# Performance work log

Measured on AMD Instinct MI355X. Metric: run time of the kernel, lower is better.

## Reference

```python
import jax, jax.numpy as jnp
import numpy as np

B, H, W, C = 32, 64, 64, 128
WIN, NH, HD = 8, 4, 32
WW = WIN * WIN          # 64 tokens per window
BW = B * (H // WIN) * (W // WIN)  # 2048 windows
LN_EPS = 1e-5


def _ln(x, w, b):
    mu = jnp.mean(x, -1, keepdims=True)
    var = jnp.var(x, -1, keepdims=True)
    return (x - mu) * jax.lax.rsqrt(var + LN_EPS) * w + b


def setup_inputs() -> dict:
    key = jax.random.key(0)
    ks = jax.random.split(key, 24)
    n = lambda i, s, sc=0.02: jax.random.normal(ks[i], s, jnp.float32) * sc
    return {
        "out_dense_b": n(0, (C,)),
        "out_dense_w": n(1, (C, C)),
        "rel_coords_table": jax.random.uniform(ks[2], (1, 2 * WIN - 1, 2 * WIN - 1, 2), jnp.float32, -1.0, 1.0),
        "cpb0_b": n(3, (512,)),
        "cpb0_w": n(4, (512, 2)),
        "cpb2_w": n(5, (NH, 512)),
        "value_b": n(6, (C,)),
        "value_w": n(7, (C, C)),
        "logit_scale": jnp.full((NH, 1, 1), jnp.log(10.0), jnp.float32),
        "inter_b": n(8, (4 * C,)),
        "inter_w": n(9, (4 * C, C)),
        "ln_after_b": n(10, (C,)),
        "ln_after_w": jnp.ones((C,), jnp.float32),
        "ln_before_b": n(11, (C,)),
        "ln_before_w": jnp.ones((C,), jnp.float32),
        "ffn_out_b": n(12, (C,)),
        "ffn_out_w": n(13, (C, 4 * C)),
        "ds_norm_b": n(14, (2 * C,)),
        "ds_norm_w": jnp.ones((2 * C,), jnp.float32),
        "ds_red_w": n(15, (2 * C, 4 * C)),
        "embeddings_3": jax.random.normal(ks[16], (B, H * W, C), jnp.float32),
        "hidden_states_windows": jax.random.normal(ks[17], (BW, WW, C), jnp.float32),
        "key_layer": jax.random.normal(ks[18], (BW, NH, WW, HD), jnp.float32),
        "query_layer": jax.random.normal(ks[19], (BW, NH, WW, HD), jnp.float32),
        "rel_pos_index": jax.random.randint(ks[20], (WW, WW), 0, (2 * WIN - 1) ** 2).astype(jnp.int64),
    }


def reference(out_dense_b, out_dense_w, rel_coords_table, cpb0_b, cpb0_w, cpb2_w,
              value_b, value_w, logit_scale, inter_b, inter_w,
              ln_after_b, ln_after_w, ln_before_b, ln_before_w,
              ffn_out_b, ffn_out_w, ds_norm_b, ds_norm_w, ds_red_w,
              embeddings_3, hidden_states_windows, key_layer, query_layer,
              rel_pos_index):
    # value projection -> [BW, NH, WW, HD]
    v = (hidden_states_windows @ value_w.T + value_b).reshape(BW, WW, NH, HD).transpose(0, 2, 1, 3)
    # cosine attention
    qn = query_layer / jnp.maximum(jnp.linalg.norm(query_layer, axis=-1, keepdims=True), 1e-12)
    kn = key_layer / jnp.maximum(jnp.linalg.norm(key_layer, axis=-1, keepdims=True), 1e-12)
    scale = jnp.exp(jnp.minimum(logit_scale, jnp.log(100.0)))  # [NH,1,1]
    attn = jnp.einsum("bhqd,bhkd->bhqk", qn, kn) * scale
    # continuous position bias MLP
    t = rel_coords_table.reshape(-1, 2)                       # [(2w-1)^2, 2]
    bias_table = jax.nn.relu(t @ cpb0_w.T + cpb0_b) @ cpb2_w.T  # [(2w-1)^2, NH]
    bias = bias_table[rel_pos_index.reshape(-1)].reshape(WW, WW, NH).transpose(2, 0, 1)
    bias = 16.0 * jax.nn.sigmoid(bias)
    attn = jax.nn.softmax(attn + bias[None], axis=-1)
    ctx = jnp.einsum("bhqk,bhkd->bhqd", attn, v).transpose(0, 2, 1, 3).reshape(BW, WW, C)
    attn_out = ctx @ out_dense_w.T + out_dense_b
    # window reverse -> [B, H*W, C]
    x = attn_out.reshape(B, H // WIN, W // WIN, WIN, WIN, C)
    x = x.transpose(0, 1, 3, 2, 4, 5).reshape(B, H * W, C)
    # res-post-norm residual
    hs = embeddings_3 + _ln(x, ln_before_w, ln_before_b)
    # MLP with res-post-norm
    ffn = jax.nn.gelu(hs @ inter_w.T + inter_b, approximate=False)
    ffn = ffn @ ffn_out_w.T + ffn_out_b
    layer_out = hs + _ln(ffn, ln_after_w, ln_after_b)
    # patch merging downsample
    xm = layer_out.reshape(B, H, W, C)
    merged = jnp.concatenate(
        [xm[:, 0::2, 0::2], xm[:, 1::2, 0::2], xm[:, 0::2, 1::2], xm[:, 1::2, 1::2]],
        axis=-1,
    ).reshape(B, (H // 2) * (W // 2), 4 * C)
    red = merged @ ds_red_w.T
    return _ln(red, ds_norm_w, ds_norm_b)
```

## Files before the change

kernel.cpp:

```cpp
#include <hip/hip_runtime.h>
#include <hip/hip_bf16.h>

typedef __attribute__((ext_vector_type(4))) float f4;
typedef __attribute__((ext_vector_type(8))) short s8;
typedef __attribute__((ext_vector_type(4))) short s4;

__device__ __forceinline__ short f2bf(float f){
  __hip_bfloat16 h = __float2bfloat16(f);
  return __builtin_bit_cast(short, h);
}
__device__ __forceinline__ float bf2f(short h){
  unsigned u = ((unsigned)(unsigned short)h) << 16;
  return __builtin_bit_cast(float, u);
}
__device__ __forceinline__ f4 mfma16(s8 a, s8 b, f4 c){
  return __builtin_amdgcn_mfma_f32_16x16x32_bf16(a, b, c, 0, 0, 0);
}
__device__ __forceinline__ s8 cfrag(const float* p){
  f4 a = *(const f4*)p; f4 b = *(const f4*)(p + 4);
  s8 t = {f2bf(a[0]), f2bf(a[1]), f2bf(a[2]), f2bf(a[3]),
          f2bf(b[0]), f2bf(b[1]), f2bf(b[2]), f2bf(b[3])};
  return t;
}
__device__ __forceinline__ s8 nfrag(const float* p){
  f4 a = *(const f4*)p; f4 b = *(const f4*)(p + 4);
  float ss = a[0]*a[0]+a[1]*a[1]+a[2]*a[2]+a[3]*a[3]
           + b[0]*b[0]+b[1]*b[1]+b[2]*b[2]+b[3]*b[3];
  ss += __shfl_xor(ss, 16); ss += __shfl_xor(ss, 32);
  float f = 1.0f / fmaxf(sqrtf(ss), 1e-12f);
  s8 t = {f2bf(a[0]*f), f2bf(a[1]*f), f2bf(a[2]*f), f2bf(a[3]*f),
          f2bf(b[0]*f), f2bf(b[1]*f), f2bf(b[2]*f), f2bf(b[3]*f)};
  return t;
}
#define SWZ(row) ((((row) ^ ((row) >> 3)) & 7) << 3)

__global__ __launch_bounds__(256) void k_prep(
    const float* __restrict__ vw, const float* __restrict__ ow,
    const float* __restrict__ iw, const float* __restrict__ fw,
    const float* __restrict__ dw, const float* __restrict__ tbl,
    const float* __restrict__ c0b, const float* __restrict__ c0w,
    const float* __restrict__ c2w, const int* __restrict__ rpi,
    short* __restrict__ wsw, float* __restrict__ bias)
{
  if (blockIdx.x < 288) {
    int e0 = (blockIdx.x * 256 + threadIdx.x) * 4;
#pragma unroll
    for (int i = 0; i < 4; ++i) {
      int e = e0 + i;
      float v;
      if (e < 16384) v = vw[e];
      else if (e < 32768) v = ow[e - 16384];
      else if (e < 98304) v = iw[e - 32768];
      else if (e < 163840) v = fw[e - 98304];
      else v = dw[e - 163840];
      wsw[e] = f2bf(v);
    }
    return;
  }
  __shared__ float tb[900];
  __shared__ float cw[1024], cb[512], c2l[2048];
  __shared__ int orAcc;
  int tid = threadIdx.x;
  if (tid == 0) orAcc = 0;
  for (int i = tid; i < 1024; i += 256) cw[i] = c0w[i];
  for (int i = tid; i < 512;  i += 256) cb[i] = c0b[i];
  for (int i = tid; i < 2048; i += 256) c2l[i] = c2w[i];
  __syncthreads();
  int my = 0;
  for (int i = tid; i < 2048; i += 256) my |= rpi[2 * i + 1];
  atomicOr(&orAcc, my);
  if (tid < 225) {
    float t0 = tbl[tid * 2 + 0], t1 = tbl[tid * 2 + 1];
    float s0 = 0.f, s1 = 0.f, s2 = 0.f, s3 = 0.f;
    for (int j = 0; j < 512; ++j) {
      float hv = fmaxf(t0 * cw[j * 2] + t1 * cw[j * 2 + 1] + cb[j], 0.f);
      s0 += hv * c2l[j];
      s1 += hv * c2l[512 + j];
      s2 += hv * c2l[1024 + j];
      s3 += hv * c2l[1536 + j];
    }
    tb[tid * 4 + 0] = s0; tb[tid * 4 + 1] = s1;
    tb[tid * 4 + 2] = s2; tb[tid * 4 + 3] = s3;
  }
  __syncthreads();
  bool i64 = (orAcc == 0);
#pragma unroll
  for (int it = 0; it < 64; ++it) {
    int e = it * 256 + tid;
    int rem = e & 4095;
    int h = e >> 12;
    int idx = i64 ? rpi[2 * rem] : rpi[rem];
    float v = tb[idx * 4 + h];
    bias[e] = 16.f / (1.f + __expf(-v));
  }
}

__global__ __launch_bounds__(256, 3) void k_attn(
    const float* __restrict__ hswp, const float* __restrict__ qg,
    const float* __restrict__ kg, const float* __restrict__ lsc,
    const float* __restrict__ vb, const short* __restrict__ wvb,
    const float* __restrict__ bias, short* __restrict__ ctx)
{
  __shared__ short lds[16384];
  const int bw = blockIdx.x, tid = threadIdx.x;
  const int lane = tid & 63, h = tid >> 6;
  const int r16 = lane & 15, b4 = lane >> 4;

  const float* qp = qg + ((size_t)bw * 4 + h) * 2048;
  const float* kp = kg + ((size_t)bw * 4 + h) * 2048;
  const float* hp = hswp + (size_t)bw * 8192;

  s8 qf[4], kf[4];
#pragma unroll
  for (int t = 0; t < 4; ++t) qf[t] = nfrag(qp + (t * 16 + r16) * 32 + b4 * 8);
#pragma unroll
  for (int t = 0; t < 4; ++t) kf[t] = nfrag(kp + (t * 16 + r16) * 32 + b4 * 8);

  {
    int row = tid >> 2, c0 = (tid & 3) * 32;
    const float* src = hp + row * 128 + c0;
    short* dst = &lds[row * 136 + c0];
#pragma unroll
    for (int j = 0; j < 4; ++j)
      *(s8*)(dst + j * 8) = cfrag(src + j * 8);
  }
  __syncthreads();

  f4 vac[2][4];
#pragma unroll
  for (int ct = 0; ct < 2; ++ct)
#pragma unroll
    for (int tt = 0; tt < 4; ++tt) vac[ct][tt] = (f4){0.f, 0.f, 0.f, 0.f};
#pragma unroll
  for (int ks = 0; ks < 4; ++ks) {
    s8 bfr[4];
#pragma unroll
    for (int tt = 0; tt < 4; ++tt)
      bfr[tt] = *(const s8*)&lds[(tt * 16 + r16) * 136 + ks * 32 + b4 * 8];
#pragma unroll
    for (int ct = 0; ct < 2; ++ct) {
      s8 af = *(const s8*)(wvb + (size_t)(h * 32 + ct * 16 + r16) * 128 + ks * 32 + b4 * 8);
#pragma unroll
      for (int tt = 0; tt < 4; ++tt)
        vac[ct][tt] = mfma16(af, bfr[tt], vac[ct][tt]);
    }
  }

  f4 sac[4][4];
#pragma unroll
  for (int a = 0; a < 4; ++a)
#pragma unroll
    for (int b = 0; b < 4; ++b) sac[a][b] = (f4){0.f, 0.f, 0.f, 0.f};
#pragma unroll
  for (int kt = 0; kt < 4; ++kt)
#pragma unroll
    for (int qt = 0; qt < 4; ++qt)
      sac[kt][qt] = mfma16(kf[kt], qf[qt], sac[kt][qt]);

  float scal = __expf(fminf(lsc[h], 4.60517019f));
  float rden[4];
#pragma unroll
  for (int qt = 0; qt < 4; ++qt) {
    float m = -1e30f;
#pragma unroll
    for (int kt = 0; kt < 4; ++kt) {
      f4 bv = *(const f4*)(bias + (h * 64 + qt * 16 + r16) * 64 + kt * 16 + b4 * 4);
#pragma unroll
      for (int r = 0; r < 4; ++r) {
        float sv = sac[kt][qt][r] * scal + bv[r];
        sac[kt][qt][r] = sv;
        m = fmaxf(m, sv);
      }
    }
    m = fmaxf(m, __shfl_xor(m, 16));
    m = fmaxf(m, __shfl_xor(m, 32));
    float sum = 0.f;
#pragma unroll
    for (int kt = 0; kt < 4; ++kt)
#pragma unroll
      for (int r = 0; r < 4; ++r) {
        float e = __expf(sac[kt][qt][r] - m);
        sac[kt][qt][r] = e;
        sum += e;
      }
    sum += __shfl_xor(sum, 16);
    sum += __shfl_xor(sum, 32);
    rden[qt] = 1.0f / sum;
  }

  __syncthreads();

  short* Vt = &lds[h * 4096];
  short* Ph = &lds[h * 4096 + 2048];

#pragma unroll
  for (int ct = 0; ct < 2; ++ct)
#pragma unroll
    for (int r = 0; r < 4; ++r) {
      int row = ct * 16 + b4 * 4 + r;
      float bvl = vb[h * 32 + row];
#pragma unroll
      for (int tt = 0; tt < 4; ++tt) {
        int col = tt * 16 + r16;
        Vt[row * 64 + (col ^ SWZ(row))] = f2bf(vac[ct][tt][r] + bvl);
      }
    }

  f4 cac[2][4];
#pragma unroll
  for (int a = 0; a < 2; ++a)
#pragma unroll
    for (int b = 0; b < 4; ++b) cac[a][b] = (f4){0.f, 0.f, 0.f, 0.f};

#pragma unroll
  for (int half = 0; half < 2; ++half) {
#pragma unroll
    for (int qt2 = 0; qt2 < 2; ++qt2) {
      int qt = half * 2 + qt2;
      int ql = qt2 * 16 + r16;
#pragma unroll
      for (int kt = 0; kt < 4; ++kt) {
        s4 p4;
#pragma unroll
        for (int r = 0; r < 4; ++r) p4[r] = f2bf(sac[kt][qt][r] * rden[qt]);
        *(s4*)&Ph[ql * 64 + ((kt * 16 + b4 * 4) ^ SWZ(ql))] = p4;
      }
    }
#pragma unroll
    for (int ks = 0; ks < 2; ++ks) {
      s8 pf[2];
#pragma unroll
      for (int qt2 = 0; qt2 < 2; ++qt2) {
        int ql = qt2 * 16 + r16;
        pf[qt2] = *(const s8*)&Ph[ql * 64 + ((ks * 32 + b4 * 8) ^ SWZ(ql))];
      }
#pragma unroll
      for (int dt = 0; dt < 2; ++dt) {
        int row = dt * 16 + r16;
        s8 vf = *(const s8*)&Vt[row * 64 + ((ks * 32 + b4 * 8) ^ SWZ(row))];
#pragma unroll
        for (int qt2 = 0; qt2 < 2; ++qt2)
          cac[dt][half * 2 + qt2] = mfma16(vf, pf[qt2], cac[dt][half * 2 + qt2]);
      }
    }
  }
#pragma unroll
  for (int qt = 0; qt < 4; ++qt)
#pragma unroll
    for (int dt = 0; dt < 2; ++dt) {
      s4 o;
#pragma unroll
      for (int r = 0; r < 4; ++r) o[r] = f2bf(cac[dt][qt][r]);
      *(s4*)(ctx + (size_t)(bw * 64 + qt * 16 + r16) * 128 + h * 32 + dt * 16 + b4 * 4) = o;
    }
}

__global__ __launch_bounds__(512, 4) void k_fuse(
    const short* __restrict__ ctx, const short* __restrict__ owb,
    const float* __restrict__ ob, const float* __restrict__ emb,
    const float* __restrict__ lnbw, const float* __restrict__ lnbb,
    const short* __restrict__ iwb, const float* __restrict__ ib,
    const short* __restrict__ fwb, const float* __restrict__ fb,
    const float* __restrict__ lnaw, const float* __restrict__ lnab,
    short* __restrict__ lo)
{
  __shared__ short Bs[128 * 136];
  __shared__ short ht[8][2184];
  const int tid = threadIdx.x, lane = tid & 63, wv = tid >> 6;
  const int r16 = lane & 15, b4 = lane >> 4;
  const int obase = blockIdx.x * 128 + wv * 16;

#pragma unroll
  for (int it = 0; it < 4; ++it) {
    int ch = it * 512 + tid, n = ch >> 4, k8 = ch & 15;
    *(s8*)&Bs[n * 136 + k8 * 8] = *(const s8*)(owb + (size_t)n * 128 + k8 * 8);
  }
  __syncthreads();

  int m = obase + r16;
  int bb = m >> 12, rimg = (m >> 6) & 63, cimg = m & 63;
  long tok = ((long)(bb * 64 + (rimg >> 3) * 8 + (cimg >> 3)) << 6)
           + (rimg & 7) * 8 + (cimg & 7);
  const short* ap = ctx + tok * 128;

  f4 acc[8];
#pragma unroll
  for (int nt = 0; nt < 8; ++nt) acc[nt] = (f4){0.f, 0.f, 0.f, 0.f};
#pragma unroll
  for (int ks = 0; ks < 4; ++ks) {
    s8 af = *(const s8*)(ap + ks * 32 + b4 * 8);
#pragma unroll
    for (int nt = 0; nt < 8; ++nt) {
      s8 bf = *(const s8*)&Bs[(nt * 16 + r16) * 136 + ks * 32 + b4 * 8];
      acc[nt] = mfma16(af, bf, acc[nt]);
    }
  }
#pragma unroll
  for (int r = 0; r < 4; ++r) {
    int t = b4 * 4 + r;
    long orow = obase + t;
    float x[8];
    float s = 0.f, s2 = 0.f;
#pragma unroll
    for (int nt = 0; nt < 8; ++nt) {
      int c = nt * 16 + r16;
      x[nt] = acc[nt][r] + ob[c];
      s += x[nt]; s2 += x[nt] * x[nt];
    }
    s += __shfl_xor(s, 1); s += __shfl_xor(s, 2); s += __shfl_xor(s, 4); s += __shfl_xor(s, 8);
    s2 += __shfl_xor(s2, 1); s2 += __shfl_xor(s2, 2); s2 += __shfl_xor(s2, 4); s2 += __shfl_xor(s2, 8);
    float mu = s * (1.f / 128.f);
    float var = s2 * (1.f / 128.f) - mu * mu;
    float rs = rsqrtf(var + 1e-5f);
#pragma unroll
    for (int nt = 0; nt < 8; ++nt) {
      int c = nt * 16 + r16;
      float y = (x[nt] - mu) * rs * lnbw[c] + lnbb[c] + emb[orow * 128 + c];
      short yb = f2bf(y);
      ht[wv][t * 136 + c] = yb;
      lo[orow * 128 + c] = yb;
    }
  }

  s8 af1[4];
#pragma unroll
  for (int ks = 0; ks < 4; ++ks)
    af1[ks] = *(const s8*)&ht[wv][r16 * 136 + ks * 32 + b4 * 8];

  f4 acc2[8];
#pragma unroll
  for (int nt = 0; nt < 8; ++nt) acc2[nt] = (f4){0.f, 0.f, 0.f, 0.f};

  for (int cc = 0; cc < 4; ++cc) {
    int n0 = cc * 128;
    __syncthreads();
#pragma unroll
    for (int it = 0; it < 4; ++it) {
      int ch = it * 512 + tid, n = ch >> 4, k8 = ch & 15;
      *(s8*)&Bs[n * 136 + k8 * 8] = *(const s8*)(iwb + (size_t)(n0 + n) * 128 + k8 * 8);
    }
    __syncthreads();
    f4 a1[8];
#pragma unroll
    for (int nt = 0; nt < 8; ++nt) a1[nt] = (f4){0.f, 0.f, 0.f, 0.f};
#pragma unroll
    for (int ks = 0; ks < 4; ++ks) {
#pragma unroll
      for (int nt = 0; nt < 8; ++nt) {
        s8 bf = *(const s8*)&Bs[(nt * 16 + r16) * 136 + ks * 32 + b4 * 8];
        a1[nt] = mfma16(af1[ks], bf, a1[nt]);
      }
    }
#pragma unroll
    for (int r = 0; r < 4; ++r) {
      int t = b4 * 4 + r;
#pragma unroll
      for (int nt = 0; nt < 8; ++nt) {
        int c = nt * 16 + r16;
        float xg = a1[nt][r] + ib[n0 + c];
        float g = 0.5f * xg * (1.0f + erff(xg * 0.70710678118f));
        ht[wv][t * 136 + c] = f2bf(g);
      }
    }
    __syncthreads();
#pragma unroll
    for (int it = 0; it < 4; ++it) {
      int ch = it * 512 + tid, n = ch >> 4, k8 = ch & 15;
      *(s8*)&Bs[n * 136 + k8 * 8] = *(const s8*)(fwb + (size_t)n * 512 + n0 + k8 * 8);
    }
    __syncthreads();
#pragma unroll
    for (int ks = 0; ks < 4; ++ks) {
      s8 af2 = *(const s8*)&ht[wv][r16 * 136 + ks * 32 + b4 * 8];
#pragma unroll
      for (int nt = 0; nt < 8; ++nt) {
        s8 bf = *(const s8*)&Bs[(nt * 16 + r16) * 136 + ks * 32 + b4 * 8];
        acc2[nt] = mfma16(af2, bf, acc2[nt]);
      }
    }
  }

#pragma unroll
  for (int r = 0; r < 4; ++r) {
    int t = b4 * 4 + r;
    long orow = obase + t;
    float x[8], res[8];
    float s = 0.f, s2 = 0.f;
#pragma unroll
    for (int nt = 0; nt < 8; ++nt) {
      int c = nt * 16 + r16;
      res[nt] = bf2f(lo[orow * 128 + c]);
      x[nt] = acc2[nt][r] + fb[c];
      s += x[nt]; s2 += x[nt] * x[nt];
    }
    s += __shfl_xor(s, 1); s += __shfl_xor(s, 2); s += __shfl_xor(s, 4); s += __shfl_xor(s, 8);
    s2 += __shfl_xor(s2, 1); s2 += __shfl_xor(s2, 2); s2 += __shfl_xor(s2, 4); s2 += __shfl_xor(s2, 8);
    float mu = s * (1.f / 128.f);
    float var = s2 * (1.f / 128.f) - mu * mu;
    float rs = rsqrtf(var + 1e-5f);
#pragma unroll
    for (int nt = 0; nt < 8; ++nt) {
      int c = nt * 16 + r16;
      float y = (x[nt] - mu) * rs * lnaw[c] + lnab[c] + res[nt];
      lo[orow * 128 + c] = f2bf(y);
    }
  }
}

__global__ __launch_bounds__(512) void k_merge(
    const short* __restrict__ lo, const short* __restrict__ dwb,
    const float* __restrict__ dsw, const float* __restrict__ dsb,
    float* __restrict__ out)
{
  __shared__ short Bs[256 * 136];
  const int tid = threadIdx.x;
  const int lane = tid & 63, wv = tid >> 6, r16 = lane & 15, b4 = lane >> 4;
  const int mrow = blockIdx.x * 128 + wv * 16;
  f4 acc[16];
#pragma unroll
  for (int nt = 0; nt < 16; ++nt) acc[nt] = (f4){0.f, 0.f, 0.f, 0.f};
  for (int kc = 0; kc < 4; ++kc) {
    if (kc) __syncthreads();
#pragma unroll
    for (int it = 0; it < 8; ++it) {
      int ch = it * 512 + tid, n = ch >> 4, k8 = ch & 15;
      *(s8*)&Bs[n * 136 + k8 * 8] = *(const s8*)(dwb + (size_t)n * 512 + kc * 128 + k8 * 8);
    }
    __syncthreads();
    int m = mrow + r16;
    int bb = m >> 10, p = m & 1023, ii = p >> 5, jj = p & 31;
    long row = (long)bb * 4096 + (2 * ii + (kc & 1)) * 64 + (2 * jj + (kc >> 1));
    const short* ap = lo + row * 128;
#pragma unroll
    for (int ks = 0; ks < 4; ++ks) {
      s8 af = *(const s8*)(ap + ks * 32 + b4 * 8);
#pragma unroll
      for (int nt = 0; nt < 16; ++nt) {
        s8 bf = *(const s8*)&Bs[(nt * 16 + r16) * 136 + ks * 32 + b4 * 8];
        acc[nt] = mfma16(af, bf, acc[nt]);
      }
    }
  }
#pragma unroll
  for (int r = 0; r < 4; ++r) {
    size_t m = mrow + b4 * 4 + r;
    float x[16];
    float s = 0.f, s2 = 0.f;
#pragma unroll
    for (int nt = 0; nt < 16; ++nt) {
      x[nt] = acc[nt][r];
      s += x[nt]; s2 += x[nt] * x[nt];
    }
    s += __shfl_xor(s, 1); s += __shfl_xor(s, 2); s += __shfl_xor(s, 4); s += __shfl_xor(s, 8);
    s2 += __shfl_xor(s2, 1); s2 += __shfl_xor(s2, 2); s2 += __shfl_xor(s2, 4); s2 += __shfl_xor(s2, 8);
    float mu = s * (1.f / 256.f);
    float var = s2 * (1.f / 256.f) - mu * mu;
    float rs = rsqrtf(var + 1e-5f);
#pragma unroll
    for (int nt = 0; nt < 16; ++nt) {
      int c = nt * 16 + r16;
      out[m * 256 + c] = (x[nt] - mu) * rs * dsw[c] + dsb[c];
    }
  }
}

extern "C" void kernel_launch(void* const* d_in, const int* in_sizes, int n_in,
                              void* d_out, int out_size, void* d_ws, size_t ws_size,
                              hipStream_t stream)
{
  const float* out_dense_b = (const float*)d_in[0];
  const float* out_dense_w = (const float*)d_in[1];
  const float* rel_tbl     = (const float*)d_in[2];
  const float* cpb0_b      = (const float*)d_in[3];
  const float* cpb0_w      = (const float*)d_in[4];
  const float* cpb2_w      = (const float*)d_in[5];
  const float* value_b     = (const float*)d_in[6];
  const float* value_w     = (const float*)d_in[7];
  const float* logit_scale = (const float*)d_in[8];
  const float* inter_b     = (const float*)d_in[9];
  const float* inter_w     = (const float*)d_in[10];
  const float* ln_after_b  = (const float*)d_in[11];
  const float* ln_after_w  = (const float*)d_in[12];
  const float* ln_before_b = (const float*)d_in[13];
  const float* ln_before_w = (const float*)d_in[14];
  const float* ffn_out_b   = (const float*)d_in[15];
  const float* ffn_out_w   = (const float*)d_in[16];
  const float* ds_norm_b   = (const float*)d_in[17];
  const float* ds_norm_w   = (const float*)d_in[18];
  const float* ds_red_w    = (const float*)d_in[19];
  const float* emb         = (const float*)d_in[20];
  const float* hsw         = (const float*)d_in[21];
  const float* keyl        = (const float*)d_in[22];
  const float* queryl      = (const float*)d_in[23];
  const int*   rpi         = (const int*)d_in[24];

  char* ws = (char*)d_ws;
  short* wsw  = (short*)ws;
  float* bias = (float*)(ws + 589824);
  short* ctx  = (short*)(ws + 655360);
  short* lo   = (short*)(ws + 655360 + 33554432ULL);

  short* wv_bf = wsw;
  short* ow_bf = wsw + 16384;
  short* iw_bf = wsw + 32768;
  short* fw_bf = wsw + 98304;
  short* dw_bf = wsw + 163840;

  k_prep<<<289, 256, 0, stream>>>(value_w, out_dense_w, inter_w, ffn_out_w, ds_red_w,
                                  rel_tbl, cpb0_b, cpb0_w, cpb2_w, rpi, wsw, bias);
  k_attn<<<2048, 256, 0, stream>>>(hsw, queryl, keyl, logit_scale, value_b, wv_bf, bias, ctx);
  k_fuse<<<1024, 512, 0, stream>>>(ctx, ow_bf, out_dense_b, emb, ln_before_w, ln_before_b,
                                   iw_bf, inter_b, fw_bf, ffn_out_b,
                                   ln_after_w, ln_after_b, lo);
  k_merge<<<256, 512, 0, stream>>>(lo, dw_bf, ds_norm_w, ds_norm_b, (float*)d_out);
}
```

Baseline: 238.9 us.

## Parallelize CPB bias table across blocks and keep residual in registers

The single-block bias preparation is split in two. The k_prep tail now computes the 225-row MLP table across 8 blocks, with 8 lanes per row reduced by shuffles. A new 16-block k_bias kernel then gathers and applies the sigmoid. Separately, k_fuse keeps the post-LN residual in registers instead of writing it to the global lo buffer and reading it back, which removes one global round trip per element. The cost is an extra kernel launch and some added register pressure.

```diff
diff --git a/kernel.cpp b/kernel.cpp
--- a/kernel.cpp
+++ b/kernel.cpp
@@ -39,11 +39,12 @@
     const float* __restrict__ iw, const float* __restrict__ fw,
     const float* __restrict__ dw, const float* __restrict__ tbl,
     const float* __restrict__ c0b, const float* __restrict__ c0w,
-    const float* __restrict__ c2w, const int* __restrict__ rpi,
-    short* __restrict__ wsw, float* __restrict__ bias)
+    const float* __restrict__ c2w,
+    short* __restrict__ wsw, float* __restrict__ tbg)
 {
+  int tid = threadIdx.x;
   if (blockIdx.x < 288) {
-    int e0 = (blockIdx.x * 256 + threadIdx.x) * 4;
+    int e0 = (blockIdx.x * 256 + tid) * 4;
 #pragma unroll
     for (int i = 0; i < 4; ++i) {
       int e = e0 + i;
@@ -57,41 +58,53 @@
     }
     return;
   }
+  int bb = blockIdx.x - 288;
+  int row = bb * 32 + (tid >> 3);
+  int k = tid & 7;
+  if (row < 225) {
+    float t0 = tbl[row * 2 + 0], t1 = tbl[row * 2 + 1];
+    float s0 = 0.f, s1 = 0.f, s2 = 0.f, s3 = 0.f;
+    int j0 = k * 64;
+    for (int j = j0; j < j0 + 64; ++j) {
+      float hv = fmaxf(t0 * c0w[j * 2] + t1 * c0w[j * 2 + 1] + c0b[j], 0.f);
+      s0 += hv * c2w[j];
+      s1 += hv * c2w[512 + j];
+      s2 += hv * c2w[1024 + j];
+      s3 += hv * c2w[1536 + j];
+    }
+    s0 += __shfl_xor(s0, 1); s0 += __shfl_xor(s0, 2); s0 += __shfl_xor(s0, 4);
+    s1 += __shfl_xor(s1, 1); s1 += __shfl_xor(s1, 2); s1 += __shfl_xor(s1, 4);
+    s2 += __shfl_xor(s2, 1); s2 += __shfl_xor(s2, 2); s2 += __shfl_xor(s2, 4);
+    s3 += __shfl_xor(s3, 1); s3 += __shfl_xor(s3, 2); s3 += __shfl_xor(s3, 4);
+    if (k == 0) {
+      tbg[row * 4 + 0] = s0; tbg[row * 4 + 1] = s1;
+      tbg[row * 4 + 2] = s2; tbg[row * 4 + 3] = s3;
+    }
+  }
+}
+
+__global__ __launch_bounds__(256) void k_bias(
+    const float* __restrict__ tbg, const int* __restrict__ rpi,
+    float* __restrict__ bias)
+{
   __shared__ float tb[900];
-  __shared__ float cw[1024], cb[512], c2l[2048];
   __shared__ int orAcc;
   int tid = threadIdx.x;
   if (tid == 0) orAcc = 0;
-  for (int i = tid; i < 1024; i += 256) cw[i] = c0w[i];
-  for (int i = tid; i < 512;  i += 256) cb[i] = c0b[i];
-  for (int i = tid; i < 2048; i += 256) c2l[i] = c2w[i];
+  for (int i = tid; i < 900; i += 256) tb[i] = tbg[i];
   __syncthreads();
   int my = 0;
   for (int i = tid; i < 2048; i += 256) my |= rpi[2 * i + 1];
   atomicOr(&orAcc, my);
-  if (tid < 225) {
-    float t0 = tbl[tid * 2 + 0], t1 = tbl[tid * 2 + 1];
-    float s0 = 0.f, s1 = 0.f, s2 = 0.f, s3 = 0.f;
-    for (int j = 0; j < 512; ++j) {
-      float hv = fmaxf(t0 * cw[j * 2] + t1 * cw[j * 2 + 1] + cb[j], 0.f);
-      s0 += hv * c2l[j];
-      s1 += hv * c2l[512 + j];
-      s2 += hv * c2l[1024 + j];
-      s3 += hv * c2l[1536 + j];
-    }
-    tb[tid * 4 + 0] = s0; tb[tid * 4 + 1] = s1;
-    tb[tid * 4 + 2] = s2; tb[tid * 4 + 3] = s3;
-  }
   __syncthreads();
   bool i64 = (orAcc == 0);
 #pragma unroll
-  for (int it = 0; it < 64; ++it) {
-    int e = it * 256 + tid;
+  for (int it = 0; it < 4; ++it) {
+    int e = blockIdx.x * 1024 + it * 256 + tid;
     int rem = e & 4095;
     int h = e >> 12;
     int idx = i64 ? rpi[2 * rem] : rpi[rem];
-    float v = tb[idx * 4 + h];
-    bias[e] = 16.f / (1.f + __expf(-v));
+    bias[e] = 16.f / (1.f + __expf(-tb[idx * 4 + h]));
   }
 }
 
@@ -295,6 +308,7 @@
       acc[nt] = mfma16(af, bf, acc[nt]);
     }
   }
+  s8 hr[4];
 #pragma unroll
   for (int r = 0; r < 4; ++r) {
     int t = b4 * 4 + r;
@@ -318,7 +332,7 @@
       float y = (x[nt] - mu) * rs * lnbw[c] + lnbb[c] + emb[orow * 128 + c];
       short yb = f2bf(y);
       ht[wv][t * 136 + c] = yb;
-      lo[orow * 128 + c] = yb;
+      hr[r][nt] = yb;
     }
   }
 
@@ -384,12 +398,11 @@
   for (int r = 0; r < 4; ++r) {
     int t = b4 * 4 + r;
     long orow = obase + t;
-    float x[8], res[8];
+    float x[8];
     float s = 0.f, s2 = 0.f;
 #pragma unroll
     for (int nt = 0; nt < 8; ++nt) {
       int c = nt * 16 + r16;
-      res[nt] = bf2f(lo[orow * 128 + c]);
       x[nt] = acc2[nt][r] + fb[c];
       s += x[nt]; s2 += x[nt] * x[nt];
     }
@@ -401,7 +414,7 @@
 #pragma unroll
     for (int nt = 0; nt < 8; ++nt) {
       int c = nt * 16 + r16;
-      float y = (x[nt] - mu) * rs * lnaw[c] + lnab[c] + res[nt];
+      float y = (x[nt] - mu) * rs * lnaw[c] + lnab[c] + bf2f(hr[r][nt]);
       lo[orow * 128 + c] = f2bf(y);
     }
   }
@@ -497,8 +510,9 @@
   char* ws = (char*)d_ws;
   short* wsw  = (short*)ws;
   float* bias = (float*)(ws + 589824);
-  short* ctx  = (short*)(ws + 655360);
-  short* lo   = (short*)(ws + 655360 + 33554432ULL);
+  float* tbg  = (float*)(ws + 655360);
+  short* ctx  = (short*)(ws + 659456);
+  short* lo   = (short*)(ws + 659456 + 33554432ULL);
 
   short* wv_bf = wsw;
   short* ow_bf = wsw + 16384;
@@ -506,8 +520,9 @@
   short* fw_bf = wsw + 98304;
   short* dw_bf = wsw + 163840;
 
-  k_prep<<<289, 256, 0, stream>>>(value_w, out_dense_w, inter_w, ffn_out_w, ds_red_w,
-                                  rel_tbl, cpb0_b, cpb0_w, cpb2_w, rpi, wsw, bias);
+  k_prep<<<296, 256, 0, stream>>>(value_w, out_dense_w, inter_w, ffn_out_w, ds_red_w,
+                                  rel_tbl, cpb0_b, cpb0_w, cpb2_w, wsw, tbg);
+  k_bias<<<16, 256, 0, stream>>>(tbg, rpi, bias);
   k_attn<<<2048, 256, 0, stream>>>(hsw, queryl, keyl, logit_scale, value_b, wv_bf, bias, ctx);
   k_fuse<<<1024, 512, 0, stream>>>(ctx, ow_bf, out_dense_b, emb, ln_before_w, ln_before_b,
                                    iw_bf, inter_b, fw_bf, ffn_out_b,
```

After: 253.0 us. +5.9%, slower.
